# Kernel tuning notes

Hardware: AMD Instinct MI355X
Metric: run time of the kernel (lower is better)

Reference implementation:

```python
import jax, jax.numpy as jnp
import numpy as np

N, E, G = 50000, 640000, 1024
D, RD, H = 128, 200, 512
NUM_ATOM_FEATS, ATOM_VOCAB = 9, 64
NUM_BOND_FEATS, BOND_VOCAB = 3, 16


def setup_inputs() -> dict:
    key = jax.random.key(0)
    ks = jax.random.split(key, 24)
    inp = {
        "x_feat": jax.random.randint(ks[0], (N, NUM_ATOM_FEATS), 0, ATOM_VOCAB),
        "edge_index": jax.random.randint(ks[1], (2, E), 0, N),
        "edge_attr_feat": jax.random.randint(ks[2], (E, NUM_BOND_FEATS), 0, BOND_VOCAB),
        "batch": jnp.sort(jax.random.randint(ks[3], (N,), 0, G)),
        "rdkit_feats": jax.random.normal(ks[4], (G, RD), dtype=jnp.float32),
        # learned params
        "atom_emb": jax.random.normal(ks[5], (NUM_ATOM_FEATS, ATOM_VOCAB, D), dtype=jnp.float32) * 0.02,
        "bond_emb": jax.random.normal(ks[6], (NUM_BOND_FEATS, BOND_VOCAB, D), dtype=jnp.float32) * 0.02,
        "conv1_w1": jax.random.normal(ks[7], (D, D), dtype=jnp.float32) / np.sqrt(D),
        "conv1_b1": jnp.zeros((D,), jnp.float32),
        "conv1_w2": jax.random.normal(ks[8], (D, D), dtype=jnp.float32) / np.sqrt(D),
        "conv1_b2": jnp.zeros((D,), jnp.float32),
        "conv2_w1": jax.random.normal(ks[9], (D, D), dtype=jnp.float32) / np.sqrt(D),
        "conv2_b1": jnp.zeros((D,), jnp.float32),
        "conv2_w2": jax.random.normal(ks[10], (D, D), dtype=jnp.float32) / np.sqrt(D),
        "conv2_b2": jnp.zeros((D,), jnp.float32),
        "mlp_w1": jax.random.normal(ks[11], (D + RD, H), dtype=jnp.float32) / np.sqrt(D + RD),
        "mlp_b1": jnp.zeros((H,), jnp.float32),
        "mlp_w2": jax.random.normal(ks[12], (H, H // 2), dtype=jnp.float32) / np.sqrt(H),
        "mlp_b2": jnp.zeros((H // 2,), jnp.float32),
        "mlp_w3": jax.random.normal(ks[13], (H // 2, 1), dtype=jnp.float32) / np.sqrt(H // 2),
        "mlp_b3": jnp.zeros((1,), jnp.float32),
    }
    return inp


def _gine_conv(x, edge_index, edge_attr, w1, b1, w2, b2, eps=0.0):
    # PyG GINEConv: out = nn((1+eps)*x + sum_{j in N(i)} relu(x_j + e_ji))
    src, dst = edge_index[0], edge_index[1]
    msg = jax.nn.relu(x[src] + edge_attr)               # [E, D]
    agg = jax.ops.segment_sum(msg, dst, num_segments=x.shape[0])  # [N, D]
    h = (1.0 + eps) * x + agg
    h = jax.nn.relu(h @ w1 + b1)
    return h @ w2 + b2


def reference(x_feat, edge_index, edge_attr_feat, batch, rdkit_feats,
              atom_emb, bond_emb,
              conv1_w1, conv1_b1, conv1_w2, conv1_b2,
              conv2_w1, conv2_b1, conv2_w2, conv2_b2,
              mlp_w1, mlp_b1, mlp_w2, mlp_b2, mlp_w3, mlp_b3):
    # AtomEncoder / BondEncoder: sum of per-feature categorical embeddings
    x = atom_emb[jnp.arange(NUM_ATOM_FEATS)[None, :], x_feat].sum(axis=1)          # [N, D]
    edge_attr = bond_emb[jnp.arange(NUM_BOND_FEATS)[None, :], edge_attr_feat].sum(axis=1)  # [E, D]

    x = _gine_conv(x, edge_index, edge_attr, conv1_w1, conv1_b1, conv1_w2, conv1_b2)
    x = _gine_conv(x, edge_index, edge_attr, conv2_w1, conv2_b1, conv2_w2, conv2_b2)

    # global mean pool over graphs
    sums = jax.ops.segment_sum(x, batch, num_segments=G)                # [G, D]
    counts = jax.ops.segment_sum(jnp.ones((x.shape[0],), x.dtype), batch, num_segments=G)
    pooled = sums / jnp.maximum(counts, 1.0)[:, None]

    h = jnp.concatenate([pooled, rdkit_feats], axis=1)                  # [G, D+RD]
    h = jax.nn.relu(h @ mlp_w1 + mlp_b1)   # dropout is identity in eval mode
    h = jax.nn.relu(h @ mlp_w2 + mlp_b2)
    return h @ mlp_w3 + mlp_b3                                          # [G, 1]
```

## Files before the change

kernel.cpp:

```cpp
#include <hip/hip_runtime.h>

#define N_NODES 50000
#define N_EDGES 640000
#define N_GRAPH 1024
#define D 128
#define RD 200

typedef __attribute__((ext_vector_type(4))) float f32x4;
typedef __attribute__((ext_vector_type(8))) float f32x8;
typedef __attribute__((ext_vector_type(2))) _Float16 half2v;
typedef __attribute__((ext_vector_type(4))) _Float16 half4;
typedef __attribute__((ext_vector_type(8))) _Float16 half8;

static __device__ __forceinline__ int lbound(const int* a, int n, int v) {
  int lo = 0, hi = n;
  while (lo < hi) { int m = (lo + hi) >> 1; if (a[m] < v) lo = m + 1; else hi = m; }
  return lo;
}

__global__ void k_prep(const float* __restrict__ w0, const float* __restrict__ w1,
                       const float* __restrict__ w2, const float* __restrict__ w3,
                       const float* __restrict__ mw1, const float* __restrict__ mw2,
                       const float* __restrict__ emb,
                       _Float16* __restrict__ cWf,
                       _Float16* __restrict__ W1f,
                       _Float16* __restrict__ W2f,
                       _Float16* __restrict__ embh,
                       int* __restrict__ deg) {
  int t = blockIdx.x * 256 + threadIdx.x;
  if (t < N_NODES) deg[t] = 0;
  if (t < 8192) {
    int mat = t >> 11, r = t & 2047;
    int frag = r >> 6, lane = r & 63;
    int n0 = frag >> 2, kk = frag & 3;
    int n = n0 * 16 + (lane & 15);
    int kb = (lane >> 4) * 8 + kk * 32;
    const float* W = (mat == 0) ? w0 : (mat == 1) ? w1 : (mat == 2) ? w2 : w3;
    half8 o;
#pragma unroll
    for (int j = 0; j < 8; ++j) o[j] = (_Float16)W[(kb + j) * D + n];
    *(half8*)&cWf[((size_t)mat * 2048 + r) * 8] = o;
  } else if (t < 8192 + 22528) {
    int u = t - 8192;
    int frag = u >> 6, lane = u & 63;
    int n0 = frag / 11, kk = frag % 11;
    int n = n0 * 16 + (lane & 15);
    int kb = (lane >> 4) * 8 + kk * 32;
    half8 o;
#pragma unroll
    for (int j = 0; j < 8; ++j) {
      int k = kb + j;
      o[j] = (k < 328) ? (_Float16)mw1[k * 512 + n] : (_Float16)0.f;
    }
    *(half8*)&W1f[(size_t)u * 8] = o;
  } else if (t < 8192 + 22528 + 16384) {
    int u = t - 8192 - 22528;
    int frag = u >> 6, lane = u & 63;
    int n0 = frag >> 4, kk = frag & 15;
    int n = n0 * 16 + (lane & 15);
    int kb = (lane >> 4) * 8 + kk * 32;
    half8 o;
#pragma unroll
    for (int j = 0; j < 8; ++j) o[j] = (_Float16)mw2[(kb + j) * 256 + n];
    *(half8*)&W2f[(size_t)u * 8] = o;
  } else if (t < 8192 + 22528 + 16384 + 9216) {
    int u = t - 8192 - 22528 - 16384;
    float4 v0 = *(const float4*)&emb[(size_t)u * 8];
    float4 v1 = *(const float4*)&emb[(size_t)u * 8 + 4];
    half8 o;
    o[0] = (_Float16)v0.x; o[1] = (_Float16)v0.y; o[2] = (_Float16)v0.z; o[3] = (_Float16)v0.w;
    o[4] = (_Float16)v1.x; o[5] = (_Float16)v1.y; o[6] = (_Float16)v1.z; o[7] = (_Float16)v1.w;
    *(half8*)&embh[(size_t)u * 8] = o;
  }
}

__global__ void k_atom_count(const int* __restrict__ xf, const _Float16* __restrict__ embh,
                             _Float16* __restrict__ x16,
                             const int* __restrict__ ei, const int* __restrict__ bondf,
                             int* __restrict__ deg,
                             int* __restrict__ dr,
                             int* __restrict__ epack) {
  if (blockIdx.x < 6250) {
    int t = blockIdx.x * 256 + threadIdx.x;
    int node = t >> 5, c = (t & 31) << 2;
    int v[9];
#pragma unroll
    for (int f = 0; f < 9; ++f) v[f] = xf[node * 9 + f];
    f32x4 a = {0.f, 0.f, 0.f, 0.f};
#pragma unroll
    for (int f = 0; f < 9; ++f) {
      half4 e4 = *(const half4*)&embh[(size_t)(f * 64 + v[f]) * D + c];
      a += __builtin_convertvector(e4, f32x4);
    }
    half4 o;
    o.x = (_Float16)a[0]; o.y = (_Float16)a[1];
    o.z = (_Float16)a[2]; o.w = (_Float16)a[3];
    *(half4*)&x16[(size_t)node * D + c] = o;
  } else {
    int e = (blockIdx.x - 6250) * 256 + threadIdx.x;
    if (e < N_EDGES) {
      int d = ei[N_EDGES + e];
      int rank = atomicAdd(&deg[d], 1);
      dr[e] = d | (rank << 16);
      int s = ei[e];
      int f0 = bondf[e * 3], f1 = bondf[e * 3 + 1], f2 = bondf[e * 3 + 2];
      epack[e] = s | (f0 << 16) | (f1 << 20) | (f2 << 24);
    }
  }
}

__global__ void k_scan_blocks(const int* __restrict__ deg, int* __restrict__ excl,
                              int* __restrict__ bsum) {
  __shared__ int sd[1024];
  int i = blockIdx.x * 1024 + threadIdx.x;
  int v = (i < N_NODES) ? deg[i] : 0;
  sd[threadIdx.x] = v;
  __syncthreads();
  for (int off = 1; off < 1024; off <<= 1) {
    int t = (threadIdx.x >= (unsigned)off) ? sd[threadIdx.x - off] : 0;
    __syncthreads();
    sd[threadIdx.x] += t;
    __syncthreads();
  }
  if (i < N_NODES) excl[i] = sd[threadIdx.x] - v;
  if (threadIdx.x == 1023) bsum[blockIdx.x] = sd[1023];
}

__global__ void k_scan_add(int* __restrict__ row_ptr, const int* __restrict__ bsum) {
  int off = 0;
  for (int b = 0; b < blockIdx.x; ++b) off += bsum[b];
  int i = blockIdx.x * 1024 + threadIdx.x;
  if (i < N_NODES) row_ptr[i] += off;
  if (blockIdx.x == 0 && threadIdx.x == 0) row_ptr[N_NODES] = N_EDGES;
}

__global__ void k_fill(const int* __restrict__ dr, const int* __restrict__ epack,
                       const int* __restrict__ row_ptr, int* __restrict__ csr1) {
  int e = blockIdx.x * 256 + threadIdx.x;
  if (e >= N_EDGES) return;
  int v = dr[e];
  int d = v & 0xFFFF, rank = v >> 16;
  csr1[row_ptr[d] + rank] = epack[e];
}

__global__ __launch_bounds__(256) void k_agg(
    const _Float16* __restrict__ x16, const int* __restrict__ row_ptr,
    const int* __restrict__ csr1, const float* __restrict__ bemb,
    _Float16* __restrict__ out) {
  __shared__ half8 sB[48 * 16];
  for (int t = threadIdx.x; t < 768; t += blockDim.x) {
    float4 v0 = *(const float4*)&bemb[t * 8];
    float4 v1 = *(const float4*)&bemb[t * 8 + 4];
    half8 h;
    h[0] = (_Float16)v0.x; h[1] = (_Float16)v0.y; h[2] = (_Float16)v0.z; h[3] = (_Float16)v0.w;
    h[4] = (_Float16)v1.x; h[5] = (_Float16)v1.y; h[6] = (_Float16)v1.z; h[7] = (_Float16)v1.w;
    sB[t] = h;
  }
  __syncthreads();
  int lane = threadIdx.x & 63;
  int quad = lane >> 4;
  int l15 = lane & 15;
  int c8 = l15 * 8;
  int wid = blockIdx.x * (blockDim.x >> 6) + (threadIdx.x >> 6);
  int nw = gridDim.x * (blockDim.x >> 6);
  for (int i = wid; i < N_NODES; i += nw) {
    f32x8 ac[2];
    ac[0] = (f32x8)(0.f); ac[1] = (f32x8)(0.f);
    int e0 = row_ptr[i], e1 = row_ptr[i + 1];
    int j = e0 + quad;
#define EDGE(u, jj)                                                          \
    {                                                                        \
      unsigned ed = (unsigned)csr1[jj];                                      \
      half8 xr = *(const half8*)&x16[(size_t)(ed & 0xFFFF) * D + c8];        \
      unsigned p = ed >> 16;                                                 \
      half8 m16 = (xr + sB[(p & 15) * 16 + l15]) +                           \
                  (sB[256 + ((p >> 4) & 15) * 16 + l15] +                    \
                   sB[512 + (p >> 8) * 16 + l15]);                           \
      f32x8 m = __builtin_convertvector(m16, f32x8);                         \
      _Pragma("unroll")                                                      \
      for (int tt = 0; tt < 8; ++tt) ac[u][tt] += fmaxf(m[tt], 0.f);         \
    }
    for (; j + 4 < e1; j += 8) { EDGE(0, j) EDGE(1, j + 4) }
    for (; j < e1; j += 4) EDGE(0, j)
#undef EDGE
    f32x8 acc = ac[0] + ac[1];
#pragma unroll
    for (int tt = 0; tt < 8; ++tt) {
      acc[tt] += __shfl_xor(acc[tt], 16);
      acc[tt] += __shfl_xor(acc[tt], 32);
    }
    if (quad == 0) {
      half8 sr = *(const half8*)&x16[(size_t)i * D + c8];
      f32x8 o = __builtin_convertvector(sr, f32x8) + acc;
      *(half8*)&out[(size_t)i * D + c8] = __builtin_convertvector(o, half8);
    }
  }
}

__global__ __launch_bounds__(256) void k_conv(
    const _Float16* __restrict__ A,
    const _Float16* __restrict__ W1f, const float* __restrict__ b1,
    const _Float16* __restrict__ W2f, const float* __restrict__ b2,
    _Float16* __restrict__ O16) {
  __shared__ _Float16 sW[2048 * 8];
  __shared__ _Float16 sI[128 * 136];
  int tid = threadIdx.x, w = tid >> 6, lane = tid & 63;
  int m0 = blockIdx.x * 128;
  int col16 = lane & 15, q = lane >> 4;
  for (int t = tid; t < 2048; t += 256)
    *(float4*)&sW[t * 8] = *(const float4*)&W1f[(size_t)t * 8];
  half8 afr[2][4];
#pragma unroll
  for (int f = 0; f < 2; ++f) {
    int row = m0 + w * 32 + f * 16 + col16;
    if (row >= N_NODES) row = N_NODES - 1;
    const _Float16* Ar = A + (size_t)row * D + q * 8;
#pragma unroll
    for (int kk = 0; kk < 4; ++kk) afr[f][kk] = *(const half8*)(Ar + kk * 32);
  }
  __syncthreads();
#pragma unroll
  for (int n0 = 0; n0 < 8; ++n0) {
    f32x4 a0 = {0.f, 0.f, 0.f, 0.f}, a1 = {0.f, 0.f, 0.f, 0.f};
#pragma unroll
    for (int kk = 0; kk < 4; ++kk) {
      half8 b = *(const half8*)&sW[((n0 * 4 + kk) * 64 + lane) * 8];
      a0 = __builtin_amdgcn_mfma_f32_16x16x32_f16(afr[0][kk], b, a0, 0, 0, 0);
      a1 = __builtin_amdgcn_mfma_f32_16x16x32_f16(afr[1][kk], b, a1, 0, 0, 0);
    }
    float bb = b1[n0 * 16 + col16];
#pragma unroll
    for (int r = 0; r < 4; ++r) {
      sI[(w * 32 + q * 4 + r) * 136 + n0 * 16 + col16] = (_Float16)fmaxf(a0[r] + bb, 0.f);
      sI[(w * 32 + 16 + q * 4 + r) * 136 + n0 * 16 + col16] = (_Float16)fmaxf(a1[r] + bb, 0.f);
    }
  }
  __syncthreads();
  for (int t = tid; t < 2048; t += 256)
    *(float4*)&sW[t * 8] = *(const float4*)&W2f[(size_t)t * 8];
  half8 a2[2][4];
#pragma unroll
  for (int f = 0; f < 2; ++f) {
    const _Float16* tr = &sI[(w * 32 + f * 16 + col16) * 136 + q * 8];
#pragma unroll
    for (int kk = 0; kk < 4; ++kk) a2[f][kk] = *(const half8*)(tr + kk * 32);
  }
  __syncthreads();
#pragma unroll
  for (int n0 = 0; n0 < 8; ++n0) {
    f32x4 a0 = {0.f, 0.f, 0.f, 0.f}, a1 = {0.f, 0.f, 0.f, 0.f};
#pragma unroll
    for (int kk = 0; kk < 4; ++kk) {
      half8 b = *(const half8*)&sW[((n0 * 4 + kk) * 64 + lane) * 8];
      a0 = __builtin_amdgcn_mfma_f32_16x16x32_f16(a2[0][kk], b, a0, 0, 0, 0);
      a1 = __builtin_amdgcn_mfma_f32_16x16x32_f16(a2[1][kk], b, a1, 0, 0, 0);
    }
    int col = n0 * 16 + col16;
    float bb = b2[col];
#pragma unroll
    for (int r = 0; r < 4; ++r) {
      int r0 = m0 + w * 32 + q * 4 + r;
      int r1 = r0 + 16;
      if (r0 < N_NODES) O16[(size_t)r0 * D + col] = (_Float16)(a0[r] + bb);
      if (r1 < N_NODES) O16[(size_t)r1 * D + col] = (_Float16)(a1[r] + bb);
    }
  }
}

__global__ __launch_bounds__(256) void k_pool(
    const _Float16* __restrict__ x, const int* __restrict__ batch,
    const float* __restrict__ rdkit, _Float16* __restrict__ hcat,
    const float* __restrict__ B3, float* __restrict__ out) {
  int g = blockIdx.x * 4 + (threadIdx.x >> 6);
  if (g >= N_GRAPH) return;
  int lane = threadIdx.x & 63;
  int half_ = lane >> 5;
  int c4 = (lane & 31) * 4;
  int lo = lbound(batch, N_NODES, g);
  int hi = lbound(batch, N_NODES, g + 1);
  f32x4 a = {0.f, 0.f, 0.f, 0.f};
  for (int i = lo + half_; i < hi; i += 2) {
    half4 v = *(const half4*)&x[(size_t)i * D + c4];
    a += __builtin_convertvector(v, f32x4);
  }
#pragma unroll
  for (int t = 0; t < 4; ++t) a[t] += __shfl_xor(a[t], 32);
  float inv = 1.f / fmaxf((float)(hi - lo), 1.f);
  if (half_ == 0) {
    half4 o;
    o.x = (_Float16)(a[0] * inv); o.y = (_Float16)(a[1] * inv);
    o.z = (_Float16)(a[2] * inv); o.w = (_Float16)(a[3] * inv);
    *(half4*)&hcat[(size_t)g * 352 + c4] = o;
  }
  for (int r = lane; r < RD; r += 64)
    hcat[(size_t)g * 352 + D + r] = (_Float16)rdkit[(size_t)g * RD + r];
  if (lane < 24) hcat[(size_t)g * 352 + 328 + lane] = (_Float16)0.f;
  if (lane == 0) out[g] = B3[0];
}

__global__ __launch_bounds__(256) void k_mlp1(
    const _Float16* __restrict__ A, const _Float16* __restrict__ W1f,
    const float* __restrict__ B, _Float16* __restrict__ O) {
  int w = threadIdx.x >> 6, lane = threadIdx.x & 63;
  int gid = blockIdx.x * 4 + w;
  int mt = gid >> 5, n0 = gid & 31;
  int col16 = lane & 15, q = lane >> 4;
  const _Float16* Ar = A + (size_t)(mt * 16 + col16) * 352 + q * 8;
  f32x4 acc = {0.f, 0.f, 0.f, 0.f};
#pragma unroll
  for (int kk = 0; kk < 11; ++kk) {
    half8 a = *(const half8*)(Ar + kk * 32);
    half8 b = *(const half8*)&W1f[(size_t)((n0 * 11 + kk) * 64 + lane) * 8];
    acc = __builtin_amdgcn_mfma_f32_16x16x32_f16(a, b, acc, 0, 0, 0);
  }
  int col = n0 * 16 + col16;
  float bb = B[col];
#pragma unroll
  for (int r = 0; r < 4; ++r) {
    int row = mt * 16 + q * 4 + r;
    O[(size_t)row * 512 + col] = (_Float16)fmaxf(acc[r] + bb, 0.f);
  }
}

__global__ __launch_bounds__(256) void k_mlp23(
    const _Float16* __restrict__ A, const _Float16* __restrict__ W2f,
    const float* __restrict__ B2, const float* __restrict__ W3,
    float* __restrict__ out) {
  int w = threadIdx.x >> 6, lane = threadIdx.x & 63;
  int gid = blockIdx.x * 4 + w;
  int mt = gid >> 4, n0 = gid & 15;
  int col16 = lane & 15, q = lane >> 4;
  const _Float16* Ar = A + (size_t)(mt * 16 + col16) * 512 + q * 8;
  f32x4 acc = {0.f, 0.f, 0.f, 0.f};
#pragma unroll
  for (int kk = 0; kk < 16; ++kk) {
    half8 a = *(const half8*)(Ar + kk * 32);
    half8 b = *(const half8*)&W2f[(size_t)((n0 * 16 + kk) * 64 + lane) * 8];
    acc = __builtin_amdgcn_mfma_f32_16x16x32_f16(a, b, acc, 0, 0, 0);
  }
  int col = n0 * 16 + col16;
  float bb = B2[col], w3 = W3[col];
  float p[4];
#pragma unroll
  for (int r = 0; r < 4; ++r) p[r] = fmaxf(acc[r] + bb, 0.f) * w3;
#pragma unroll
  for (int r = 0; r < 4; ++r) {
    p[r] += __shfl_xor(p[r], 1);
    p[r] += __shfl_xor(p[r], 2);
    p[r] += __shfl_xor(p[r], 4);
    p[r] += __shfl_xor(p[r], 8);
  }
  if (col16 == 0) {
#pragma unroll
    for (int r = 0; r < 4; ++r)
      atomicAdd(&out[mt * 16 + q * 4 + r], p[r]);
  }
}

extern "C" void kernel_launch(void* const* d_in, const int* in_sizes, int n_in,
                              void* d_out, int out_size, void* d_ws, size_t ws_size,
                              hipStream_t stream) {
  const int* x_feat = (const int*)d_in[0];
  const int* ei = (const int*)d_in[1];
  const int* bondf = (const int*)d_in[2];
  const int* batch = (const int*)d_in[3];
  const float* rdkit = (const float*)d_in[4];
  const float* atom_emb = (const float*)d_in[5];
  const float* bond_emb = (const float*)d_in[6];
  const float* c1w1 = (const float*)d_in[7];
  const float* c1b1 = (const float*)d_in[8];
  const float* c1w2 = (const float*)d_in[9];
  const float* c1b2 = (const float*)d_in[10];
  const float* c2w1 = (const float*)d_in[11];
  const float* c2b1 = (const float*)d_in[12];
  const float* c2w2 = (const float*)d_in[13];
  const float* c2b2 = (const float*)d_in[14];
  const float* mw1 = (const float*)d_in[15];
  const float* mb1 = (const float*)d_in[16];
  const float* mw2 = (const float*)d_in[17];
  const float* mb2 = (const float*)d_in[18];
  const float* mw3 = (const float*)d_in[19];
  const float* mb3 = (const float*)d_in[20];
  float* out = (float*)d_out;

  char* ws = (char*)d_ws;
  size_t off = 0;
  auto alloc = [&](size_t bytes) {
    void* p = ws + off;
    off += (bytes + 255) & ~(size_t)255;
    return p;
  };
  _Float16* x16a = (_Float16*)alloc((size_t)N_NODES * D * 2);
  _Float16* x16b = (_Float16*)alloc((size_t)N_NODES * D * 2);
  _Float16* h16 = (_Float16*)alloc((size_t)N_NODES * D * 2);
  _Float16* x2_16 = (_Float16*)alloc((size_t)N_NODES * D * 2);
  int* deg = (int*)alloc((size_t)N_NODES * 4);
  int* row_ptr = (int*)alloc((size_t)(N_NODES + 1) * 4);
  int* bsum = (int*)alloc(64 * 4);
  int* csr1 = (int*)alloc((size_t)N_EDGES * 4);
  int* dr = (int*)alloc((size_t)N_EDGES * 4);
  int* epack = (int*)alloc((size_t)N_EDGES * 4);
  _Float16* hcat16 = (_Float16*)alloc((size_t)N_GRAPH * 352 * 2);
  _Float16* h1buf = (_Float16*)alloc((size_t)N_GRAPH * 512 * 2);
  _Float16* cWf = (_Float16*)alloc((size_t)4 * 2048 * 8 * 2);
  _Float16* W1f = (_Float16*)alloc((size_t)352 * 64 * 8 * 2);
  _Float16* W2f = (_Float16*)alloc((size_t)256 * 64 * 8 * 2);
  _Float16* embh = (_Float16*)alloc((size_t)9 * 64 * D * 2);

  k_prep<<<256, 256, 0, stream>>>(c1w1, c1w2, c2w1, c2w2, mw1, mw2, atom_emb,
                                  cWf, W1f, W2f, embh, deg);
  k_atom_count<<<6250 + 2500, 256, 0, stream>>>(x_feat, embh, x16a,
                                                ei, bondf, deg, dr, epack);

  int nb = (N_NODES + 1023) / 1024;
  k_scan_blocks<<<nb, 1024, 0, stream>>>(deg, row_ptr, bsum);
  k_scan_add<<<nb, 1024, 0, stream>>>(row_ptr, bsum);
  k_fill<<<(N_EDGES + 255) / 256, 256, 0, stream>>>(dr, epack, row_ptr, csr1);

  int ctiles = (N_NODES + 127) / 128;
  k_agg<<<2048, 256, 0, stream>>>(x16a, row_ptr, csr1, bond_emb, h16);
  k_conv<<<ctiles, 256, 0, stream>>>(h16, cWf + 0 * 16384, c1b1,
                                     cWf + 1 * 16384, c1b2, x16b);
  k_agg<<<2048, 256, 0, stream>>>(x16b, row_ptr, csr1, bond_emb, h16);
  k_conv<<<ctiles, 256, 0, stream>>>(h16, cWf + 2 * 16384, c2b1,
                                     cWf + 3 * 16384, c2b2, x2_16);

  k_pool<<<N_GRAPH / 4, 256, 0, stream>>>(x2_16, batch, rdkit, hcat16, mb3, out);
  k_mlp1<<<512, 256, 0, stream>>>(hcat16, W1f, mb1, h1buf);
  k_mlp23<<<256, 256, 0, stream>>>(h1buf, W2f, mb2, mw3, out);

  (void)in_sizes; (void)n_in; (void)out_size; (void)ws_size;
}
```

Before: 284.5 us.

## Fuse edge aggregation into conv MLP kernel and pack CSR build buffers

```diff
diff --git a/kernel.cpp b/kernel.cpp
--- a/kernel.cpp
+++ b/kernel.cpp
@@ -78,33 +78,31 @@
                              _Float16* __restrict__ x16,
                              const int* __restrict__ ei, const int* __restrict__ bondf,
                              int* __restrict__ deg,
-                             int* __restrict__ dr,
-                             int* __restrict__ epack) {
-  if (blockIdx.x < 6250) {
+                             int2* __restrict__ drep) {
+  if (blockIdx.x < 3125) {
     int t = blockIdx.x * 256 + threadIdx.x;
-    int node = t >> 5, c = (t & 31) << 2;
+    int node = t >> 4, c = (t & 15) << 3;
     int v[9];
 #pragma unroll
     for (int f = 0; f < 9; ++f) v[f] = xf[node * 9 + f];
-    f32x4 a = {0.f, 0.f, 0.f, 0.f};
+    f32x8 a = (f32x8)(0.f);
 #pragma unroll
     for (int f = 0; f < 9; ++f) {
-      half4 e4 = *(const half4*)&embh[(size_t)(f * 64 + v[f]) * D + c];
-      a += __builtin_convertvector(e4, f32x4);
-    }
-    half4 o;
-    o.x = (_Float16)a[0]; o.y = (_Float16)a[1];
-    o.z = (_Float16)a[2]; o.w = (_Float16)a[3];
-    *(half4*)&x16[(size_t)node * D + c] = o;
+      half8 e8 = *(const half8*)&embh[(size_t)(f * 64 + v[f]) * D + c];
+      a += __builtin_convertvector(e8, f32x8);
+    }
+    half8 o;
+#pragma unroll
+    for (int tt = 0; tt < 8; ++tt) o[tt] = (_Float16)a[tt];
+    *(half8*)&x16[(size_t)node * D + c] = o;
   } else {
-    int e = (blockIdx.x - 6250) * 256 + threadIdx.x;
+    int e = (blockIdx.x - 3125) * 256 + threadIdx.x;
     if (e < N_EDGES) {
       int d = ei[N_EDGES + e];
       int rank = atomicAdd(&deg[d], 1);
-      dr[e] = d | (rank << 16);
       int s = ei[e];
       int f0 = bondf[e * 3], f1 = bondf[e * 3 + 1], f2 = bondf[e * 3 + 2];
-      epack[e] = s | (f0 << 16) | (f1 << 20) | (f2 << 24);
+      drep[e] = make_int2(d | (rank << 16), s | (f0 << 16) | (f1 << 20) | (f2 << 24));
     }
   }
 }
@@ -127,28 +125,46 @@
 }
 
 __global__ void k_scan_add(int* __restrict__ row_ptr, const int* __restrict__ bsum) {
-  int off = 0;
-  for (int b = 0; b < blockIdx.x; ++b) off += bsum[b];
+  __shared__ int s_off;
+  if (threadIdx.x < 64) {
+    int v = ((int)threadIdx.x < (int)blockIdx.x) ? bsum[threadIdx.x] : 0;
+#pragma unroll
+    for (int o = 1; o < 64; o <<= 1) v += __shfl_xor(v, o);
+    if (threadIdx.x == 0) s_off = v;
+  }
+  __syncthreads();
+  int off = s_off;
   int i = blockIdx.x * 1024 + threadIdx.x;
   if (i < N_NODES) row_ptr[i] += off;
   if (blockIdx.x == 0 && threadIdx.x == 0) row_ptr[N_NODES] = N_EDGES;
 }
 
-__global__ void k_fill(const int* __restrict__ dr, const int* __restrict__ epack,
+__global__ void k_fill(const int2* __restrict__ drep,
                        const int* __restrict__ row_ptr, int* __restrict__ csr1) {
   int e = blockIdx.x * 256 + threadIdx.x;
   if (e >= N_EDGES) return;
-  int v = dr[e];
-  int d = v & 0xFFFF, rank = v >> 16;
-  csr1[row_ptr[d] + rank] = epack[e];
-}
-
-__global__ __launch_bounds__(256) void k_agg(
-    const _Float16* __restrict__ x16, const int* __restrict__ row_ptr,
+  int2 v = drep[e];
+  int d = v.x & 0xFFFF;
+  int rank = ((unsigned)v.x) >> 16;
+  csr1[row_ptr[d] + rank] = v.y;
+}
+
+__global__ __launch_bounds__(256, 2) void k_aggconv(
+    const _Float16* __restrict__ X, const int* __restrict__ row_ptr,
     const int* __restrict__ csr1, const float* __restrict__ bemb,
-    _Float16* __restrict__ out) {
+    const _Float16* __restrict__ W1f, const float* __restrict__ b1,
+    const _Float16* __restrict__ W2f, const float* __restrict__ b2,
+    _Float16* __restrict__ O16) {
+  __shared__ _Float16 sW[2048 * 8];
+  __shared__ _Float16 sI[128 * 136];
   __shared__ half8 sB[48 * 16];
-  for (int t = threadIdx.x; t < 768; t += blockDim.x) {
+  int tid = threadIdx.x, w = tid >> 6, lane = tid & 63;
+  int m0 = blockIdx.x * 128;
+  int quad = lane >> 4, l15 = lane & 15, c8 = l15 * 8;
+
+  for (int t = tid; t < 2048; t += 256)
+    *(float4*)&sW[t * 8] = *(const float4*)&W1f[(size_t)t * 8];
+  for (int t = tid; t < 768; t += 256) {
     float4 v0 = *(const float4*)&bemb[t * 8];
     float4 v1 = *(const float4*)&bemb[t * 8 + 4];
     half8 h;
@@ -157,68 +173,77 @@
     sB[t] = h;
   }
   __syncthreads();
-  int lane = threadIdx.x & 63;
-  int quad = lane >> 4;
-  int l15 = lane & 15;
-  int c8 = l15 * 8;
-  int wid = blockIdx.x * (blockDim.x >> 6) + (threadIdx.x >> 6);
-  int nw = gridDim.x * (blockDim.x >> 6);
-  for (int i = wid; i < N_NODES; i += nw) {
-    f32x8 ac[2];
-    ac[0] = (f32x8)(0.f); ac[1] = (f32x8)(0.f);
-    int e0 = row_ptr[i], e1 = row_ptr[i + 1];
-    int j = e0 + quad;
-#define EDGE(u, jj)                                                          \
-    {                                                                        \
-      unsigned ed = (unsigned)csr1[jj];                                      \
-      half8 xr = *(const half8*)&x16[(size_t)(ed & 0xFFFF) * D + c8];        \
-      unsigned p = ed >> 16;                                                 \
-      half8 m16 = (xr + sB[(p & 15) * 16 + l15]) +                           \
-                  (sB[256 + ((p >> 4) & 15) * 16 + l15] +                    \
-                   sB[512 + (p >> 8) * 16 + l15]);                           \
-      f32x8 m = __builtin_convertvector(m16, f32x8);                         \
-      _Pragma("unroll")                                                      \
-      for (int tt = 0; tt < 8; ++tt) ac[u][tt] += fmaxf(m[tt], 0.f);         \
-    }
-    for (; j + 4 < e1; j += 8) { EDGE(0, j) EDGE(1, j + 4) }
-    for (; j < e1; j += 4) EDGE(0, j)
-#undef EDGE
-    f32x8 acc = ac[0] + ac[1];
+
+  int base = m0 + w * 32;
+  int rp = 0;
+  {
+    int idx = base + lane;
+    if (lane <= 32) rp = row_ptr[idx > N_NODES ? N_NODES : idx];
+  }
+  for (int n = 0; n < 32; ++n) {
+    int i = base + n;
+    if (i >= N_NODES) break;
+    int e0 = __shfl(rp, n), e1 = __shfl(rp, n + 1);
+    int degn = e1 - e0;
+    int dq = degn > 64 ? 64 : degn;
+    int creg = (lane < dq) ? csr1[e0 + lane] : 0;
+    f32x8 ac0 = (f32x8)(0.f), ac1 = (f32x8)(0.f);
+    for (int jb = 0; jb < dq; jb += 8) {
+      unsigned e0v = (unsigned)__shfl(creg, jb + quad);
+      unsigned e1v = (unsigned)__shfl(creg, jb + 4 + quad);
+      if (jb + quad < dq) {
+        half8 x0 = *(const half8*)&X[(size_t)(e0v & 0xFFFF) * D + c8];
+        unsigned p0 = e0v >> 16;
+        half8 m0h = (x0 + sB[(p0 & 15) * 16 + l15]) +
+                    (sB[256 + ((p0 >> 4) & 15) * 16 + l15] + sB[512 + (p0 >> 8) * 16 + l15]);
+        f32x8 g0 = __builtin_convertvector(m0h, f32x8);
+#pragma unroll
+        for (int tt = 0; tt < 8; ++tt) ac0[tt] += fmaxf(g0[tt], 0.f);
+      }
+      if (jb + 4 + quad < dq) {
+        half8 x1 = *(const half8*)&X[(size_t)(e1v & 0xFFFF) * D + c8];
+        unsigned p1 = e1v >> 16;
+        half8 m1h = (x1 + sB[(p1 & 15) * 16 + l15]) +
+                    (sB[256 + ((p1 >> 4) & 15) * 16 + l15] + sB[512 + (p1 >> 8) * 16 + l15]);
+        f32x8 g1 = __builtin_convertvector(m1h, f32x8);
+#pragma unroll
+        for (int tt = 0; tt < 8; ++tt) ac1[tt] += fmaxf(g1[tt], 0.f);
+      }
+    }
+    for (int jj = e0 + 64 + quad; jj < e1; jj += 4) {
+      unsigned ev = (unsigned)csr1[jj];
+      half8 x0 = *(const half8*)&X[(size_t)(ev & 0xFFFF) * D + c8];
+      unsigned p0 = ev >> 16;
+      half8 m0h = (x0 + sB[(p0 & 15) * 16 + l15]) +
+                  (sB[256 + ((p0 >> 4) & 15) * 16 + l15] + sB[512 + (p0 >> 8) * 16 + l15]);
+      f32x8 g0 = __builtin_convertvector(m0h, f32x8);
+#pragma unroll
+      for (int tt = 0; tt < 8; ++tt) ac0[tt] += fmaxf(g0[tt], 0.f);
+    }
+    f32x8 acc = ac0 + ac1;
 #pragma unroll
     for (int tt = 0; tt < 8; ++tt) {
       acc[tt] += __shfl_xor(acc[tt], 16);
       acc[tt] += __shfl_xor(acc[tt], 32);
     }
     if (quad == 0) {
-      half8 sr = *(const half8*)&x16[(size_t)i * D + c8];
+      half8 sr = *(const half8*)&X[(size_t)i * D + c8];
       f32x8 o = __builtin_convertvector(sr, f32x8) + acc;
-      *(half8*)&out[(size_t)i * D + c8] = __builtin_convertvector(o, half8);
-    }
-  }
-}
-
-__global__ __launch_bounds__(256) void k_conv(
-    const _Float16* __restrict__ A,
-    const _Float16* __restrict__ W1f, const float* __restrict__ b1,
-    const _Float16* __restrict__ W2f, const float* __restrict__ b2,
-    _Float16* __restrict__ O16) {
-  __shared__ _Float16 sW[2048 * 8];
-  __shared__ _Float16 sI[128 * 136];
-  int tid = threadIdx.x, w = tid >> 6, lane = tid & 63;
-  int m0 = blockIdx.x * 128;
-  int col16 = lane & 15, q = lane >> 4;
-  for (int t = tid; t < 2048; t += 256)
-    *(float4*)&sW[t * 8] = *(const float4*)&W1f[(size_t)t * 8];
+      half8 oh;
+#pragma unroll
+      for (int tt = 0; tt < 8; ++tt) oh[tt] = (_Float16)o[tt];
+      *(half8*)&sI[(size_t)(w * 32 + n) * 136 + c8] = oh;
+    }
+  }
+
+  int col16 = l15, q = quad;
   half8 afr[2][4];
 #pragma unroll
   for (int f = 0; f < 2; ++f) {
-    int row = m0 + w * 32 + f * 16 + col16;
-    if (row >= N_NODES) row = N_NODES - 1;
-    const _Float16* Ar = A + (size_t)row * D + q * 8;
+    const _Float16* Ar = &sI[(size_t)(w * 32 + f * 16 + col16) * 136 + q * 8];
 #pragma unroll
     for (int kk = 0; kk < 4; ++kk) afr[f][kk] = *(const half8*)(Ar + kk * 32);
   }
-  __syncthreads();
 #pragma unroll
   for (int n0 = 0; n0 < 8; ++n0) {
     f32x4 a0 = {0.f, 0.f, 0.f, 0.f}, a1 = {0.f, 0.f, 0.f, 0.f};
@@ -241,7 +266,7 @@
   half8 a2[2][4];
 #pragma unroll
   for (int f = 0; f < 2; ++f) {
-    const _Float16* tr = &sI[(w * 32 + f * 16 + col16) * 136 + q * 8];
+    const _Float16* tr = &sI[(size_t)(w * 32 + f * 16 + col16) * 136 + q * 8];
 #pragma unroll
     for (int kk = 0; kk < 4; ++kk) a2[f][kk] = *(const half8*)(tr + kk * 32);
   }
@@ -392,14 +417,12 @@
   };
   _Float16* x16a = (_Float16*)alloc((size_t)N_NODES * D * 2);
   _Float16* x16b = (_Float16*)alloc((size_t)N_NODES * D * 2);
-  _Float16* h16 = (_Float16*)alloc((size_t)N_NODES * D * 2);
   _Float16* x2_16 = (_Float16*)alloc((size_t)N_NODES * D * 2);
   int* deg = (int*)alloc((size_t)N_NODES * 4);
   int* row_ptr = (int*)alloc((size_t)(N_NODES + 1) * 4);
   int* bsum = (int*)alloc(64 * 4);
   int* csr1 = (int*)alloc((size_t)N_EDGES * 4);
-  int* dr = (int*)alloc((size_t)N_EDGES * 4);
-  int* epack = (int*)alloc((size_t)N_EDGES * 4);
+  int2* drep = (int2*)alloc((size_t)N_EDGES * 8);
   _Float16* hcat16 = (_Float16*)alloc((size_t)N_GRAPH * 352 * 2);
   _Float16* h1buf = (_Float16*)alloc((size_t)N_GRAPH * 512 * 2);
   _Float16* cWf = (_Float16*)alloc((size_t)4 * 2048 * 8 * 2);
@@ -409,21 +432,21 @@
 
   k_prep<<<256, 256, 0, stream>>>(c1w1, c1w2, c2w1, c2w2, mw1, mw2, atom_emb,
                                   cWf, W1f, W2f, embh, deg);
-  k_atom_count<<<6250 + 2500, 256, 0, stream>>>(x_feat, embh, x16a,
-                                                ei, bondf, deg, dr, epack);
+  k_atom_count<<<3125 + 2500, 256, 0, stream>>>(x_feat, embh, x16a,
+                                                ei, bondf, deg, drep);
 
   int nb = (N_NODES + 1023) / 1024;
   k_scan_blocks<<<nb, 1024, 0, stream>>>(deg, row_ptr, bsum);
   k_scan_add<<<nb, 1024, 0, stream>>>(row_ptr, bsum);
-  k_fill<<<(N_EDGES + 255) / 256, 256, 0, stream>>>(dr, epack, row_ptr, csr1);
+  k_fill<<<(N_EDGES + 255) / 256, 256, 0, stream>>>(drep, row_ptr, csr1);
 
   int ctiles = (N_NODES + 127) / 128;
-  k_agg<<<2048, 256, 0, stream>>>(x16a, row_ptr, csr1, bond_emb, h16);
-  k_conv<<<ctiles, 256, 0, stream>>>(h16, cWf + 0 * 16384, c1b1,
-                                     cWf + 1 * 16384, c1b2, x16b);
-  k_agg<<<2048, 256, 0, stream>>>(x16b, row_ptr, csr1, bond_emb, h16);
-  k_conv<<<ctiles, 256, 0, stream>>>(h16, cWf + 2 * 16384, c2b1,
-                                     cWf + 3 * 16384, c2b2, x2_16);
+  k_aggconv<<<ctiles, 256, 0, stream>>>(x16a, row_ptr, csr1, bond_emb,
+                                        cWf + 0 * 16384, c1b1,
+                                        cWf + 1 * 16384, c1b2, x16b);
+  k_aggconv<<<ctiles, 256, 0, stream>>>(x16b, row_ptr, csr1, bond_emb,
+                                        cWf + 2 * 16384, c2b1,
+                                        cWf + 3 * 16384, c2b2, x2_16);
 
   k_pool<<<N_GRAPH / 4, 256, 0, stream>>>(x2_16, batch, rdkit, hcat16, mb3, out);
   k_mlp1<<<512, 256, 0, stream>>>(hcat16, W1f, mb1, h1buf);
```

Result: slower. 374.9 us (+31.8%).
